# Kernel tuning notes

Measured on AMD Instinct MI355X. Metric: run time of the kernel, lower is better.

Reference implementation:

```python
import jax, jax.numpy as jnp
import numpy as np

ALPHA = 0.2  # LeakyReLU negative slope
NEG_INF = -9e15


def setup_inputs() -> dict:
    key = jax.random.key(0)
    ks = jax.random.split(key, 9)
    B, N, Fin, Fout, H = 4, 1024, 256, 256, 32
    h = jax.random.normal(ks[0], (B, N, Fin), dtype=jnp.float32)
    mz = jax.random.uniform(ks[1], (B, N, 1), dtype=jnp.float32) * 2000.0
    adj = jax.random.randint(ks[2], (B, N, N), 0, 2, dtype=jnp.int32)
    # xavier_uniform with gain=1.414
    def xavier(k, shape, gain=1.414):
        fan_in, fan_out = shape[0], shape[1]
        bound = gain * np.sqrt(6.0 / (fan_in + fan_out))
        return jax.random.uniform(k, shape, jnp.float32, -bound, bound)
    W = xavier(ks[3], (Fin, Fout))
    a = xavier(ks[4], (2 * Fout, 1))
    w1 = xavier(ks[5], (1, H), gain=1.0)
    b1 = jnp.zeros((H,), jnp.float32)
    w2 = xavier(ks[6], (H, 1), gain=1.0)
    b2 = jnp.zeros((1,), jnp.float32)
    return {"h": h, "mz": mz, "W": W, "a": a, "w1": w1, "b1": b1, "w2": w2, "b2": b2, "adj": adj}


def reference(h, mz, W, a, w1, b1, w2, b2, adj):
    # h: (B,N,Fin), mz: (B,N,1), adj: (B,N,N)
    Wh = jnp.matmul(h, W)                       # (B,N,Fout)
    Fout = W.shape[1]
    a1 = a[:Fout, 0]                            # (Fout,)
    a2 = a[Fout:, 0]                            # (Fout,)
    # e[b,i,j] = leaky_relu(Wh[b,i]@a1 + Wh[b,j]@a2)  (identical to concat trick)
    s1 = jnp.einsum('bnf,f->bn', Wh, a1)
    s2 = jnp.einsum('bnf,f->bn', Wh, a2)
    e = jax.nn.leaky_relu(s1[:, :, None] + s2[:, None, :], negative_slope=ALPHA)  # (B,N,N)
    # |mz_i - mz_j| with first row/col zeroed
    diff = jnp.abs(mz - jnp.swapaxes(mz, 1, 2))  # (B,N,N)
    diff = diff.at[:, 0, :].set(0.0)
    diff = diff.at[:, :, 0].set(0.0)
    # tiny per-edge MLP: Linear(1,32)->ReLU->Linear(32,1)
    hdn = jax.nn.relu(diff[..., None] * w1[0] + b1)       # (B,N,N,32)
    diff_term = jnp.einsum('bijh,h->bij', hdn, w2[:, 0]) + b2[0]
    e = e + diff_term
    att = jnp.where(adj > 0, e, NEG_INF)
    att = jax.nn.softmax(att, axis=2)
    # dropout is identity in eval mode
    h_prime = jnp.matmul(att, Wh)               # (B,N,Fout)
    return jax.nn.elu(h_prime)
```

## Files before the change

kernel.cpp:

```cpp
#include <hip/hip_runtime.h>
#include <hip/hip_bf16.h>

#define ALPHA 0.2f
#define NEGINF -9000000000000000.0f

typedef __attribute__((ext_vector_type(8))) short short8;
typedef __attribute__((ext_vector_type(4))) float f32x4;
typedef __attribute__((ext_vector_type(4))) int i32x4;
typedef __attribute__((ext_vector_type(4))) unsigned short u16x4;

static constexpr int NB = 4, NN = 1024, NF = 256, NH = 32;

__device__ __forceinline__ unsigned short f2bf(float x) {
  union { float f; unsigned u; } v; v.f = x;
  unsigned r = v.u + 0x7fffu + ((v.u >> 16) & 1u);
  return (unsigned short)(r >> 16);
}

__global__ __launch_bounds__(256) void prep_kernel(
    const float* __restrict__ W, const float* __restrict__ a,
    const float* __restrict__ w1, const float* __restrict__ b1,
    const float* __restrict__ w2, const float* __restrict__ b2,
    float* __restrict__ wa1, float* __restrict__ wa2,
    unsigned short* __restrict__ WTp, float* __restrict__ seg) {
  int k = blockIdx.x;
  int t = threadIdx.x;
  float w = W[k * NF + t];
  WTp[(((k >> 3) * NF) + t) * 8 + (k & 7)] = f2bf(w);
  float p1 = w * a[t];
  float p2 = w * a[NF + t];
#pragma unroll
  for (int off = 32; off >= 1; off >>= 1) {
    p1 += __shfl_xor(p1, off);
    p2 += __shfl_xor(p2, off);
  }
  __shared__ float r1[4], r2[4];
  int wid = t >> 6;
  if ((t & 63) == 0) { r1[wid] = p1; r2[wid] = p2; }
  __syncthreads();
  if (t == 0) {
    wa1[k] = r1[0] + r1[1] + r1[2] + r1[3];
    wa2[k] = r2[0] + r2[1] + r2[2] + r2[3];
  }
  if (k == 0 && t < NH) {
    float w1h = w1[t], b1h = b1[t], w2h = w2[t];
    bool bp = (w1h != 0.f) && (b1h != 0.f) && ((b1h > 0.f) != (w1h > 0.f));
    bool act = (w1h + b1h) > 0.f;
    float cA = act ? w2h * w1h : 0.f;
    float cB = act ? w2h * b1h : 0.f;
    float nbp = bp ? 1.f : 0.f;
#pragma unroll
    for (int off = 16; off >= 1; off >>= 1) {
      cA += __shfl_xor(cA, off);
      cB += __shfl_xor(cB, off);
      nbp += __shfl_xor(nbp, off);
    }
    if (t == 0) {
      seg[0] = (nbp == 0.f) ? 1.f : 0.f;
      seg[1] = cA;
      seg[2] = cB + b2[0];
      seg[3] = 0.f;
    }
  }
}

__global__ __launch_bounds__(512) void wh_kernel(
    const float* __restrict__ h, const unsigned short* __restrict__ WTp,
    const float* __restrict__ wa1, const float* __restrict__ wa2,
    unsigned short* __restrict__ WhP, float* __restrict__ s1g,
    float* __restrict__ s2g) {
  __shared__ unsigned short hs[16 * 256];
  int bid = blockIdx.x;
  int b = bid >> 6;
  int rb = (bid & 63) << 4;
  int t = threadIdx.x;
  {
    int row = t >> 5, c0 = (t & 31) * 8;
    const float* src = h + (size_t)(b * NN + rb + row) * NF + c0;
    f32x4 v0 = *(const f32x4*)src;
    f32x4 v1 = *(const f32x4*)(src + 4);
    unsigned short tmp[8] = {f2bf(v0.x), f2bf(v0.y), f2bf(v0.z), f2bf(v0.w),
                             f2bf(v1.x), f2bf(v1.y), f2bf(v1.z), f2bf(v1.w)};
    int off = row * 512 + ((c0 * 2) ^ ((row & 7) << 4));
    *(short8*)((char*)hs + off) = *(const short8*)tmp;
    f32x4 a10 = *(const f32x4*)(wa1 + c0);
    f32x4 a11 = *(const f32x4*)(wa1 + c0 + 4);
    f32x4 a20 = *(const f32x4*)(wa2 + c0);
    f32x4 a21 = *(const f32x4*)(wa2 + c0 + 4);
    float d1 = v0.x * a10.x + v0.y * a10.y + v0.z * a10.z + v0.w * a10.w +
               v1.x * a11.x + v1.y * a11.y + v1.z * a11.z + v1.w * a11.w;
    float d2 = v0.x * a20.x + v0.y * a20.y + v0.z * a20.z + v0.w * a20.w +
               v1.x * a21.x + v1.y * a21.y + v1.z * a21.z + v1.w * a21.w;
#pragma unroll
    for (int off2 = 16; off2 >= 1; off2 >>= 1) {
      d1 += __shfl_xor(d1, off2);
      d2 += __shfl_xor(d2, off2);
    }
    if ((t & 31) == 0) {
      s1g[b * NN + rb + row] = d1;
      s2g[b * NN + rb + row] = d2;
    }
  }
  __syncthreads();
  int wid = t >> 6, lane = t & 63;
  int fb = wid * 32;
  int rowa = lane & 15, kg = lane >> 4;
  f32x4 acc0 = {0.f, 0.f, 0.f, 0.f}, acc1 = {0.f, 0.f, 0.f, 0.f};
#pragma unroll
  for (int ks = 0; ks < 8; ++ks) {
    int k0 = ks * 32;
    short8 af = *(const short8*)((const char*)hs + rowa * 512 +
                                 ((2 * (k0 + kg * 8)) ^ ((rowa & 7) << 4)));
    int kc = ks * 4 + kg;
    short8 bf0 = *(const short8*)(WTp + ((kc * NF) + fb + (lane & 15)) * 8);
    short8 bf1 = *(const short8*)(WTp + ((kc * NF) + fb + 16 + (lane & 15)) * 8);
    acc0 = __builtin_amdgcn_mfma_f32_16x16x32_bf16(af, bf0, acc0, 0, 0, 0);
    acc1 = __builtin_amdgcn_mfma_f32_16x16x32_bf16(af, bf1, acc1, 0, 0, 0);
  }
#pragma unroll
  for (int r = 0; r < 4; ++r) {
    int jl = (lane >> 4) * 4 + r;
    int j = rb + jl;
    int base = ((b << 7) + (j >> 3)) * NF;
    WhP[(size_t)(base + fb + (lane & 15)) * 8 + (j & 7)] = f2bf(acc0[r]);
    WhP[(size_t)(base + fb + 16 + (lane & 15)) * 8 + (j & 7)] = f2bf(acc1[r]);
  }
}

__global__ __launch_bounds__(512) void attn_kernel(
    const float* __restrict__ s1g, const float* __restrict__ s2g,
    const float* __restrict__ mz, const int* __restrict__ adj,
    const unsigned short* __restrict__ WhP,
    const float* __restrict__ w1, const float* __restrict__ b1,
    const float* __restrict__ w2, const float* __restrict__ b2,
    const float* __restrict__ seg, float* __restrict__ out) {
  __shared__ unsigned short Pb[16 * 1024];
  __shared__ float s2s[1024];
  __shared__ float mzs[1024];
  __shared__ float s1s[16];
  __shared__ float rinv[16];
  int bid0 = blockIdx.x;
  int bid = (bid0 & 7) * 32 + (bid0 >> 3);
  int b = bid >> 6;
  int rb = (bid & 63) << 4;
  int t = threadIdx.x;
  for (int i = t; i < NN; i += 512) {
    s2s[i] = s2g[b * NN + i];
    mzs[i] = mz[b * NN + i];
  }
  if (t < 16) s1s[t] = s1g[b * NN + rb + t];
  __syncthreads();

  int wid = t >> 6, lane = t & 63;
  float segF = seg[0], segA = seg[1], segB = seg[2];
  float b2v = b2[0];
  for (int rr = 0; rr < 2; ++rr) {
    int row = wid * 2 + rr;
    int ig = rb + row;
    float s1v = s1s[row];
    float mzi = mzs[ig];
    const int* adjrow = adj + ((size_t)b * NN + ig) * NN;
    float e[16];
    if (segF != 0.f) {
#pragma unroll
      for (int c = 0; c < 4; ++c) {
        int j0 = c * 256 + lane * 4;
        i32x4 av = *(const i32x4*)(adjrow + j0);
        f32x4 mzv = *(const f32x4*)(mzs + j0);
        f32x4 s2v = *(const f32x4*)(s2s + j0);
#pragma unroll
        for (int u = 0; u < 4; ++u) {
          float dd = fabsf(mzi - mzv[u]);
          float d = (ig == 0 || (j0 + u) == 0) ? 0.f : dd;
          float s = s1v + s2v[u];
          s = fmaxf(s, 0.f) + ALPHA * fminf(s, 0.f);
          float ee = s + fmaf(d, segA, segB);
          e[c * 4 + u] = (av[u] > 0) ? ee : NEGINF;
        }
      }
    } else {
#pragma unroll
      for (int c = 0; c < 4; ++c) {
        int j0 = c * 256 + lane * 4;
        i32x4 av = *(const i32x4*)(adjrow + j0);
        f32x4 mzv = *(const f32x4*)(mzs + j0);
        f32x4 s2v = *(const f32x4*)(s2s + j0);
        float d[4], acc[4];
#pragma unroll
        for (int u = 0; u < 4; ++u) {
          float dd = fabsf(mzi - mzv[u]);
          d[u] = (ig == 0 || (j0 + u) == 0) ? 0.f : dd;
          acc[u] = b2v;
        }
#pragma unroll
        for (int hh = 0; hh < NH; ++hh) {
          float w1h = w1[hh], b1h = b1[hh], w2h = w2[hh];
#pragma unroll
          for (int u = 0; u < 4; ++u)
            acc[u] += fmaxf(d[u] * w1h + b1h, 0.f) * w2h;
        }
#pragma unroll
        for (int u = 0; u < 4; ++u) {
          float s = s1v + s2v[u];
          s = s > 0.f ? s : ALPHA * s;
          e[c * 4 + u] = (av[u] > 0) ? (s + acc[u]) : NEGINF;
        }
      }
    }
    float m = -3.0e38f;
#pragma unroll
    for (int q = 0; q < 16; ++q) m = fmaxf(m, e[q]);
#pragma unroll
    for (int off = 32; off >= 1; off >>= 1) m = fmaxf(m, __shfl_xor(m, off));
    float sum = 0.f;
#pragma unroll
    for (int q = 0; q < 16; ++q) {
      e[q] = __expf(e[q] - m);
      sum += e[q];
    }
#pragma unroll
    for (int off = 32; off >= 1; off >>= 1) sum += __shfl_xor(sum, off);
#pragma unroll
    for (int c = 0; c < 4; ++c) {
      u16x4 pk = {f2bf(e[c * 4 + 0]), f2bf(e[c * 4 + 1]),
                  f2bf(e[c * 4 + 2]), f2bf(e[c * 4 + 3])};
      int byteoff = row * 2048 + ((512 * c + 8 * lane) ^ ((row & 7) << 4));
      *(u16x4*)((char*)Pb + byteoff) = pk;
    }
    if (lane == 0) rinv[row] = 1.0f / sum;
  }
  __syncthreads();

  int fb = wid * 32;
  int rowa = lane & 15, kg = lane >> 4;
  const unsigned short* whb = WhP + (((size_t)b) << 7) * NF * 8;
  f32x4 acc0 = {0.f, 0.f, 0.f, 0.f}, acc1 = {0.f, 0.f, 0.f, 0.f};
#pragma unroll 4
  for (int ks = 0; ks < 32; ++ks) {
    int k0 = ks * 32;
    short8 af = *(const short8*)((const char*)Pb + rowa * 2048 +
                                 ((2 * (k0 + kg * 8)) ^ ((rowa & 7) << 4)));
    int kc = ks * 4 + kg;
    short8 bf0 = *(const short8*)(whb + (size_t)((kc * NF) + fb + (lane & 15)) * 8);
    short8 bf1 = *(const short8*)(whb + (size_t)((kc * NF) + fb + 16 + (lane & 15)) * 8);
    acc0 = __builtin_amdgcn_mfma_f32_16x16x32_bf16(af, bf0, acc0, 0, 0, 0);
    acc1 = __builtin_amdgcn_mfma_f32_16x16x32_bf16(af, bf1, acc1, 0, 0, 0);
  }
#pragma unroll
  for (int r = 0; r < 4; ++r) {
    int il = (lane >> 4) * 4 + r;
    float inv = rinv[il];
    float x0 = acc0[r] * inv;
    float x1 = acc1[r] * inv;
    x0 = x0 > 0.f ? x0 : expm1f(x0);
    x1 = x1 > 0.f ? x1 : expm1f(x1);
    size_t ob = (size_t)(b * NN + rb + il) * NF + fb + (lane & 15);
    out[ob] = x0;
    out[ob + 16] = x1;
  }
}

extern "C" void kernel_launch(void* const* d_in, const int* in_sizes, int n_in,
                              void* d_out, int out_size, void* d_ws, size_t ws_size,
                              hipStream_t stream) {
  const float* h   = (const float*)d_in[0];
  const float* mz  = (const float*)d_in[1];
  const float* W   = (const float*)d_in[2];
  const float* a   = (const float*)d_in[3];
  const float* w1  = (const float*)d_in[4];
  const float* b1  = (const float*)d_in[5];
  const float* w2  = (const float*)d_in[6];
  const float* b2  = (const float*)d_in[7];
  const int*   adj = (const int*)d_in[8];
  float* out = (float*)d_out;

  unsigned short* WTp = (unsigned short*)d_ws;
  unsigned short* WhP = WTp + 65536;
  float* wa1 = (float*)(WhP + (size_t)NB * 128 * NF * 8);
  float* wa2 = wa1 + 256;
  float* s1g = wa2 + 256;
  float* s2g = s1g + NB * NN;
  float* segb = s2g + NB * NN;

  prep_kernel<<<dim3(256), dim3(256), 0, stream>>>(W, a, w1, b1, w2, b2,
                                                   wa1, wa2, WTp, segb);
  wh_kernel<<<dim3(256), dim3(512), 0, stream>>>(h, WTp, wa1, wa2, WhP, s1g, s2g);
  attn_kernel<<<dim3(256), dim3(512), 0, stream>>>(s1g, s2g, mz, adj, WhP,
                                                   w1, b1, w2, b2, segb, out);
}
```

Measured before the change: 28.95 us.

## Fuse three kernels into one persistent kernel with grid barriers

Merges the prep, Wh projection and attention kernels into a single 256-block kernel that uses atomic-counter grid barriers between phases, removing two kernel launches and their gaps. The adjacency rows are prefetched into registers before the second barrier so their load overlaps the barrier wait. s1 stays in shared memory instead of going through global memory, and ELU uses __expf-1 instead of expm1f. The grid barrier assumes all 256 blocks are co-resident, adds a memset launch to reset the counter, and costs extra register pressure from the prefetched adjacency data.

```diff
diff --git a/kernel.cpp b/kernel.cpp
--- a/kernel.cpp
+++ b/kernel.cpp
@@ -9,7 +9,7 @@
 typedef __attribute__((ext_vector_type(4))) int i32x4;
 typedef __attribute__((ext_vector_type(4))) unsigned short u16x4;
 
-static constexpr int NB = 4, NN = 1024, NF = 256, NH = 32;
+static constexpr int NB = 4, NN = 1024, NF = 256, NH = 32, NGRID = 256;
 
 __device__ __forceinline__ unsigned short f2bf(float x) {
   union { float f; unsigned u; } v; v.f = x;
@@ -17,63 +17,86 @@
   return (unsigned short)(r >> 16);
 }
 
-__global__ __launch_bounds__(256) void prep_kernel(
+__device__ __forceinline__ void grid_barrier(unsigned* cnt) {
+  __syncthreads();
+  if (threadIdx.x == 0) {
+    __hip_atomic_fetch_add(cnt, 1u, __ATOMIC_ACQ_REL, __HIP_MEMORY_SCOPE_AGENT);
+    while (__hip_atomic_load(cnt, __ATOMIC_ACQUIRE, __HIP_MEMORY_SCOPE_AGENT) <
+           (unsigned)NGRID)
+      __builtin_amdgcn_s_sleep(2);
+  }
+  __syncthreads();
+}
+
+__global__ __launch_bounds__(512) void fused_kernel(
+    const float* __restrict__ h, const float* __restrict__ mz,
     const float* __restrict__ W, const float* __restrict__ a,
     const float* __restrict__ w1, const float* __restrict__ b1,
     const float* __restrict__ w2, const float* __restrict__ b2,
+    const int* __restrict__ adj,
+    unsigned short* __restrict__ WTp, unsigned short* __restrict__ WhP,
     float* __restrict__ wa1, float* __restrict__ wa2,
-    unsigned short* __restrict__ WTp, float* __restrict__ seg) {
-  int k = blockIdx.x;
-  int t = threadIdx.x;
-  float w = W[k * NF + t];
-  WTp[(((k >> 3) * NF) + t) * 8 + (k & 7)] = f2bf(w);
-  float p1 = w * a[t];
-  float p2 = w * a[NF + t];
-#pragma unroll
-  for (int off = 32; off >= 1; off >>= 1) {
-    p1 += __shfl_xor(p1, off);
-    p2 += __shfl_xor(p2, off);
-  }
+    float* __restrict__ s2g, unsigned* __restrict__ bar,
+    float* __restrict__ out) {
+  __shared__ char smemraw[32 * 1024];
+  __shared__ float mzs[1024];
+  __shared__ float s2s[1024];
+  __shared__ float s1s[16];
+  __shared__ float rinv[16];
   __shared__ float r1[4], r2[4];
-  int wid = t >> 6;
-  if ((t & 63) == 0) { r1[wid] = p1; r2[wid] = p2; }
-  __syncthreads();
-  if (t == 0) {
-    wa1[k] = r1[0] + r1[1] + r1[2] + r1[3];
-    wa2[k] = r2[0] + r2[1] + r2[2] + r2[3];
-  }
-  if (k == 0 && t < NH) {
-    float w1h = w1[t], b1h = b1[t], w2h = w2[t];
-    bool bp = (w1h != 0.f) && (b1h != 0.f) && ((b1h > 0.f) != (w1h > 0.f));
-    bool act = (w1h + b1h) > 0.f;
-    float cA = act ? w2h * w1h : 0.f;
-    float cB = act ? w2h * b1h : 0.f;
-    float nbp = bp ? 1.f : 0.f;
-#pragma unroll
-    for (int off = 16; off >= 1; off >>= 1) {
-      cA += __shfl_xor(cA, off);
-      cB += __shfl_xor(cB, off);
-      nbp += __shfl_xor(nbp, off);
-    }
-    if (t == 0) {
-      seg[0] = (nbp == 0.f) ? 1.f : 0.f;
-      seg[1] = cA;
-      seg[2] = cB + b2[0];
-      seg[3] = 0.f;
-    }
-  }
-}
-
-__global__ __launch_bounds__(512) void wh_kernel(
-    const float* __restrict__ h, const unsigned short* __restrict__ WTp,
-    const float* __restrict__ wa1, const float* __restrict__ wa2,
-    unsigned short* __restrict__ WhP, float* __restrict__ s1g,
-    float* __restrict__ s2g) {
-  __shared__ unsigned short hs[16 * 256];
-  int bid = blockIdx.x;
+  __shared__ float segsh[3];
+
+  int bid0 = blockIdx.x;
+  int bid = (bid0 & 7) * 32 + (bid0 >> 3);
   int b = bid >> 6;
   int rb = (bid & 63) << 4;
   int t = threadIdx.x;
+  int wid = t >> 6, lane = t & 63;
+
+  {
+    int k = bid0;
+    float p1 = 0.f, p2 = 0.f;
+    if (t < 256) {
+      float w = W[k * NF + t];
+      WTp[(((k >> 3) * NF) + t) * 8 + (k & 7)] = f2bf(w);
+      p1 = w * a[t];
+      p2 = w * a[NF + t];
+    }
+#pragma unroll
+    for (int off = 32; off >= 1; off >>= 1) {
+      p1 += __shfl_xor(p1, off);
+      p2 += __shfl_xor(p2, off);
+    }
+    if (t < 256 && (t & 63) == 0) { r1[t >> 6] = p1; r2[t >> 6] = p2; }
+    if (t < NH) {
+      float w1h = w1[t], b1h = b1[t], w2h = w2[t];
+      bool bp = (w1h != 0.f) && (b1h != 0.f) && ((b1h > 0.f) != (w1h > 0.f));
+      bool act = (w1h + b1h) > 0.f;
+      float cA = act ? w2h * w1h : 0.f;
+      float cB = act ? w2h * b1h : 0.f;
+      float nbp = bp ? 1.f : 0.f;
+#pragma unroll
+      for (int off = 16; off >= 1; off >>= 1) {
+        cA += __shfl_xor(cA, off);
+        cB += __shfl_xor(cB, off);
+        nbp += __shfl_xor(nbp, off);
+      }
+      if (t == 0) {
+        segsh[0] = (nbp == 0.f) ? 1.f : 0.f;
+        segsh[1] = cA;
+        segsh[2] = cB + b2[0];
+      }
+    }
+    for (int i = t; i < NN; i += 512) mzs[i] = mz[b * NN + i];
+    __syncthreads();
+    if (t == 0) {
+      wa1[k] = r1[0] + r1[1] + r1[2] + r1[3];
+      wa2[k] = r2[0] + r2[1] + r2[2] + r2[3];
+    }
+  }
+  grid_barrier(bar + 0);
+
+  unsigned short* hs = (unsigned short*)smemraw;
   {
     int row = t >> 5, c0 = (t & 31) * 8;
     const float* src = h + (size_t)(b * NN + rb + row) * NF + c0;
@@ -97,75 +120,67 @@
       d2 += __shfl_xor(d2, off2);
     }
     if ((t & 31) == 0) {
-      s1g[b * NN + rb + row] = d1;
+      s1s[row] = d1;
       s2g[b * NN + rb + row] = d2;
     }
   }
   __syncthreads();
-  int wid = t >> 6, lane = t & 63;
-  int fb = wid * 32;
-  int rowa = lane & 15, kg = lane >> 4;
-  f32x4 acc0 = {0.f, 0.f, 0.f, 0.f}, acc1 = {0.f, 0.f, 0.f, 0.f};
-#pragma unroll
-  for (int ks = 0; ks < 8; ++ks) {
-    int k0 = ks * 32;
-    short8 af = *(const short8*)((const char*)hs + rowa * 512 +
-                                 ((2 * (k0 + kg * 8)) ^ ((rowa & 7) << 4)));
-    int kc = ks * 4 + kg;
-    short8 bf0 = *(const short8*)(WTp + ((kc * NF) + fb + (lane & 15)) * 8);
-    short8 bf1 = *(const short8*)(WTp + ((kc * NF) + fb + 16 + (lane & 15)) * 8);
-    acc0 = __builtin_amdgcn_mfma_f32_16x16x32_bf16(af, bf0, acc0, 0, 0, 0);
-    acc1 = __builtin_amdgcn_mfma_f32_16x16x32_bf16(af, bf1, acc1, 0, 0, 0);
-  }
-#pragma unroll
-  for (int r = 0; r < 4; ++r) {
-    int jl = (lane >> 4) * 4 + r;
-    int j = rb + jl;
-    int base = ((b << 7) + (j >> 3)) * NF;
-    WhP[(size_t)(base + fb + (lane & 15)) * 8 + (j & 7)] = f2bf(acc0[r]);
-    WhP[(size_t)(base + fb + 16 + (lane & 15)) * 8 + (j & 7)] = f2bf(acc1[r]);
-  }
-}
-
-__global__ __launch_bounds__(512) void attn_kernel(
-    const float* __restrict__ s1g, const float* __restrict__ s2g,
-    const float* __restrict__ mz, const int* __restrict__ adj,
-    const unsigned short* __restrict__ WhP,
-    const float* __restrict__ w1, const float* __restrict__ b1,
-    const float* __restrict__ w2, const float* __restrict__ b2,
-    const float* __restrict__ seg, float* __restrict__ out) {
-  __shared__ unsigned short Pb[16 * 1024];
-  __shared__ float s2s[1024];
-  __shared__ float mzs[1024];
-  __shared__ float s1s[16];
-  __shared__ float rinv[16];
-  int bid0 = blockIdx.x;
-  int bid = (bid0 & 7) * 32 + (bid0 >> 3);
-  int b = bid >> 6;
-  int rb = (bid & 63) << 4;
-  int t = threadIdx.x;
-  for (int i = t; i < NN; i += 512) {
-    s2s[i] = s2g[b * NN + i];
-    mzs[i] = mz[b * NN + i];
-  }
-  if (t < 16) s1s[t] = s1g[b * NN + rb + t];
-  __syncthreads();
-
-  int wid = t >> 6, lane = t & 63;
-  float segF = seg[0], segA = seg[1], segB = seg[2];
+  {
+    int fb = wid * 32;
+    int rowa = lane & 15, kg = lane >> 4;
+    f32x4 acc0 = {0.f, 0.f, 0.f, 0.f}, acc1 = {0.f, 0.f, 0.f, 0.f};
+#pragma unroll
+    for (int ks = 0; ks < 8; ++ks) {
+      int k0 = ks * 32;
+      short8 af = *(const short8*)((const char*)hs + rowa * 512 +
+                                   ((2 * (k0 + kg * 8)) ^ ((rowa & 7) << 4)));
+      int kc = ks * 4 + kg;
+      short8 bf0 = *(const short8*)(WTp + ((kc * NF) + fb + (lane & 15)) * 8);
+      short8 bf1 = *(const short8*)(WTp + ((kc * NF) + fb + 16 + (lane & 15)) * 8);
+      acc0 = __builtin_amdgcn_mfma_f32_16x16x32_bf16(af, bf0, acc0, 0, 0, 0);
+      acc1 = __builtin_amdgcn_mfma_f32_16x16x32_bf16(af, bf1, acc1, 0, 0, 0);
+    }
+#pragma unroll
+    for (int r = 0; r < 4; ++r) {
+      int jl = (lane >> 4) * 4 + r;
+      int j = rb + jl;
+      int base = ((b << 7) + (j >> 3)) * NF;
+      WhP[(size_t)(base + fb + (lane & 15)) * 8 + (j & 7)] = f2bf(acc0[r]);
+      WhP[(size_t)(base + fb + 16 + (lane & 15)) * 8 + (j & 7)] = f2bf(acc1[r]);
+    }
+  }
+
+  i32x4 adjreg[8];
+  {
+    const int* adjb = adj + (size_t)b * NN * NN;
+#pragma unroll
+    for (int rr = 0; rr < 2; ++rr) {
+      int ig = rb + wid * 2 + rr;
+#pragma unroll
+      for (int c = 0; c < 4; ++c)
+        adjreg[rr * 4 + c] =
+            *(const i32x4*)(adjb + (size_t)ig * NN + c * 256 + lane * 4);
+    }
+  }
+  grid_barrier(bar + 1);
+
+  unsigned short* Pb = (unsigned short*)smemraw;
+  for (int i = t; i < NN; i += 512) s2s[i] = s2g[b * NN + i];
+  __syncthreads();
+
+  float segF = segsh[0], segA = segsh[1], segB = segsh[2];
   float b2v = b2[0];
   for (int rr = 0; rr < 2; ++rr) {
     int row = wid * 2 + rr;
     int ig = rb + row;
     float s1v = s1s[row];
     float mzi = mzs[ig];
-    const int* adjrow = adj + ((size_t)b * NN + ig) * NN;
     float e[16];
     if (segF != 0.f) {
 #pragma unroll
       for (int c = 0; c < 4; ++c) {
         int j0 = c * 256 + lane * 4;
-        i32x4 av = *(const i32x4*)(adjrow + j0);
+        i32x4 av = adjreg[rr * 4 + c];
         f32x4 mzv = *(const f32x4*)(mzs + j0);
         f32x4 s2v = *(const f32x4*)(s2s + j0);
 #pragma unroll
@@ -182,7 +197,7 @@
 #pragma unroll
       for (int c = 0; c < 4; ++c) {
         int j0 = c * 256 + lane * 4;
-        i32x4 av = *(const i32x4*)(adjrow + j0);
+        i32x4 av = adjreg[rr * 4 + c];
         f32x4 mzv = *(const f32x4*)(mzs + j0);
         f32x4 s2v = *(const f32x4*)(s2s + j0);
         float d[4], acc[4];
@@ -231,32 +246,35 @@
   }
   __syncthreads();
 
-  int fb = wid * 32;
-  int rowa = lane & 15, kg = lane >> 4;
-  const unsigned short* whb = WhP + (((size_t)b) << 7) * NF * 8;
-  f32x4 acc0 = {0.f, 0.f, 0.f, 0.f}, acc1 = {0.f, 0.f, 0.f, 0.f};
+  {
+    int fb = wid * 32;
+    int rowa = lane & 15, kg = lane >> 4;
+    const unsigned short* whb = WhP + (((size_t)b) << 7) * NF * 8;
+    f32x4 acc0 = {0.f, 0.f, 0.f, 0.f}, acc1 = {0.f, 0.f, 0.f, 0.f};
 #pragma unroll 4
-  for (int ks = 0; ks < 32; ++ks) {
-    int k0 = ks * 32;
-    short8 af = *(const short8*)((const char*)Pb + rowa * 2048 +
-                                 ((2 * (k0 + kg * 8)) ^ ((rowa & 7) << 4)));
-    int kc = ks * 4 + kg;
-    short8 bf0 = *(const short8*)(whb + (size_t)((kc * NF) + fb + (lane & 15)) * 8);
-    short8 bf1 = *(const short8*)(whb + (size_t)((kc * NF) + fb + 16 + (lane & 15)) * 8);
-    acc0 = __builtin_amdgcn_mfma_f32_16x16x32_bf16(af, bf0, acc0, 0, 0, 0);
-    acc1 = __builtin_amdgcn_mfma_f32_16x16x32_bf16(af, bf1, acc1, 0, 0, 0);
-  }
-#pragma unroll
-  for (int r = 0; r < 4; ++r) {
-    int il = (lane >> 4) * 4 + r;
-    float inv = rinv[il];
-    float x0 = acc0[r] * inv;
-    float x1 = acc1[r] * inv;
-    x0 = x0 > 0.f ? x0 : expm1f(x0);
-    x1 = x1 > 0.f ? x1 : expm1f(x1);
-    size_t ob = (size_t)(b * NN + rb + il) * NF + fb + (lane & 15);
-    out[ob] = x0;
-    out[ob + 16] = x1;
+    for (int ks = 0; ks < 32; ++ks) {
+      int k0 = ks * 32;
+      short8 af = *(const short8*)((const char*)Pb + rowa * 2048 +
+                                   ((2 * (k0 + kg * 8)) ^ ((rowa & 7) << 4)));
+      int kc = ks * 4 + kg;
+      short8 bf0 = *(const short8*)(whb + (size_t)((kc * NF) + fb + (lane & 15)) * 8);
+      short8 bf1 =
+          *(const short8*)(whb + (size_t)((kc * NF) + fb + 16 + (lane & 15)) * 8);
+      acc0 = __builtin_amdgcn_mfma_f32_16x16x32_bf16(af, bf0, acc0, 0, 0, 0);
+      acc1 = __builtin_amdgcn_mfma_f32_16x16x32_bf16(af, bf1, acc1, 0, 0, 0);
+    }
+#pragma unroll
+    for (int r = 0; r < 4; ++r) {
+      int il = (lane >> 4) * 4 + r;
+      float inv = rinv[il];
+      float x0 = acc0[r] * inv;
+      float x1 = acc1[r] * inv;
+      x0 = x0 > 0.f ? x0 : (__expf(x0) - 1.f);
+      x1 = x1 > 0.f ? x1 : (__expf(x1) - 1.f);
+      size_t ob = (size_t)(b * NN + rb + il) * NF + fb + (lane & 15);
+      out[ob] = x0;
+      out[ob + 16] = x1;
+    }
   }
 }
 
@@ -276,15 +294,12 @@
 
   unsigned short* WTp = (unsigned short*)d_ws;
   unsigned short* WhP = WTp + 65536;
-  float* wa1 = (float*)(WhP + (size_t)NB * 128 * NF * 8);
+  float* wa1 = (float*)(WhP + (size_t)NB * NN * NF);
   float* wa2 = wa1 + 256;
-  float* s1g = wa2 + 256;
-  float* s2g = s1g + NB * NN;
-  float* segb = s2g + NB * NN;
-
-  prep_kernel<<<dim3(256), dim3(256), 0, stream>>>(W, a, w1, b1, w2, b2,
-                                                   wa1, wa2, WTp, segb);
-  wh_kernel<<<dim3(256), dim3(512), 0, stream>>>(h, WTp, wa1, wa2, WhP, s1g, s2g);
-  attn_kernel<<<dim3(256), dim3(512), 0, stream>>>(s1g, s2g, mz, adj, WhP,
-                                                   w1, b1, w2, b2, segb, out);
+  float* s2g = wa2 + 256;
+  unsigned* bar = (unsigned*)(s2g + NB * NN);
+
+  (void)hipMemsetAsync(bar, 0, 2 * sizeof(unsigned), stream);
+  fused_kernel<<<dim3(NGRID), dim3(512), 0, stream>>>(
+      h, mz, W, a, w1, b1, w2, b2, adj, WTp, WhP, wa1, wa2, s2g, bar, out);
 }
```

After: 63.51 us. 119% more time.

## Use 32-row attention tiles with 1024 threads and prefetch adjacency into registers

Applied to the files above, without the earlier changes.

The attention kernel now handles 32 query rows per block with 1024 threads over 128 blocks. Each wave's MFMA step reuses one Wh B-fragment across two 16-row P tiles, halving global B loads per output. Adjacency rows are loaded into registers at kernel start to overlap with the shared-memory staging, and the MLP segment precompute moves from the prep kernel into each attention block. The risks are only 128 blocks on a 256-CU part, higher register pressure, and redundant per-block precompute.

```diff
diff --git a/kernel.cpp b/kernel.cpp
--- a/kernel.cpp
+++ b/kernel.cpp
@@ -19,10 +19,8 @@
 
 __global__ __launch_bounds__(256) void prep_kernel(
     const float* __restrict__ W, const float* __restrict__ a,
-    const float* __restrict__ w1, const float* __restrict__ b1,
-    const float* __restrict__ w2, const float* __restrict__ b2,
     float* __restrict__ wa1, float* __restrict__ wa2,
-    unsigned short* __restrict__ WTp, float* __restrict__ seg) {
+    unsigned short* __restrict__ WTp) {
   int k = blockIdx.x;
   int t = threadIdx.x;
   float w = W[k * NF + t];
@@ -35,32 +33,11 @@
     p2 += __shfl_xor(p2, off);
   }
   __shared__ float r1[4], r2[4];
-  int wid = t >> 6;
-  if ((t & 63) == 0) { r1[wid] = p1; r2[wid] = p2; }
+  if ((t & 63) == 0) { r1[t >> 6] = p1; r2[t >> 6] = p2; }
   __syncthreads();
   if (t == 0) {
     wa1[k] = r1[0] + r1[1] + r1[2] + r1[3];
     wa2[k] = r2[0] + r2[1] + r2[2] + r2[3];
-  }
-  if (k == 0 && t < NH) {
-    float w1h = w1[t], b1h = b1[t], w2h = w2[t];
-    bool bp = (w1h != 0.f) && (b1h != 0.f) && ((b1h > 0.f) != (w1h > 0.f));
-    bool act = (w1h + b1h) > 0.f;
-    float cA = act ? w2h * w1h : 0.f;
-    float cB = act ? w2h * b1h : 0.f;
-    float nbp = bp ? 1.f : 0.f;
-#pragma unroll
-    for (int off = 16; off >= 1; off >>= 1) {
-      cA += __shfl_xor(cA, off);
-      cB += __shfl_xor(cB, off);
-      nbp += __shfl_xor(nbp, off);
-    }
-    if (t == 0) {
-      seg[0] = (nbp == 0.f) ? 1.f : 0.f;
-      seg[1] = cA;
-      seg[2] = cB + b2[0];
-      seg[3] = 0.f;
-    }
   }
 }
 
@@ -127,45 +104,77 @@
   }
 }
 
-__global__ __launch_bounds__(512) void attn_kernel(
-    const float* __restrict__ s1g, const float* __restrict__ s2g,
+__global__ __launch_bounds__(1024) void attn_kernel(
     const float* __restrict__ mz, const int* __restrict__ adj,
     const unsigned short* __restrict__ WhP,
     const float* __restrict__ w1, const float* __restrict__ b1,
     const float* __restrict__ w2, const float* __restrict__ b2,
-    const float* __restrict__ seg, float* __restrict__ out) {
-  __shared__ unsigned short Pb[16 * 1024];
+    const float* __restrict__ s1g, const float* __restrict__ s2g,
+    float* __restrict__ out) {
+  __shared__ unsigned short Pb[32 * 1024];
+  __shared__ float mzs[1024];
   __shared__ float s2s[1024];
-  __shared__ float mzs[1024];
-  __shared__ float s1s[16];
-  __shared__ float rinv[16];
+  __shared__ float s1s[32];
+  __shared__ float rinv[32];
+  __shared__ float segsh[3];
+
   int bid0 = blockIdx.x;
-  int bid = (bid0 & 7) * 32 + (bid0 >> 3);
-  int b = bid >> 6;
-  int rb = (bid & 63) << 4;
+  int bid = (bid0 & 7) * 16 + (bid0 >> 3);
+  int b = bid >> 5;
+  int rb = (bid & 31) << 5;
   int t = threadIdx.x;
-  for (int i = t; i < NN; i += 512) {
-    s2s[i] = s2g[b * NN + i];
-    mzs[i] = mz[b * NN + i];
-  }
-  if (t < 16) s1s[t] = s1g[b * NN + rb + t];
-  __syncthreads();
-
   int wid = t >> 6, lane = t & 63;
-  float segF = seg[0], segA = seg[1], segB = seg[2];
+
+  i32x4 adjreg[8];
+  {
+    const int* adjb = adj + (size_t)b * NN * NN;
+#pragma unroll
+    for (int rr = 0; rr < 2; ++rr) {
+      int ig = rb + wid * 2 + rr;
+#pragma unroll
+      for (int c = 0; c < 4; ++c)
+        adjreg[rr * 4 + c] =
+            *(const i32x4*)(adjb + (size_t)ig * NN + c * 256 + lane * 4);
+    }
+  }
+
+  if (t < NH) {
+    float w1h = w1[t], b1h = b1[t], w2h = w2[t];
+    bool bp = (w1h != 0.f) && (b1h != 0.f) && ((b1h > 0.f) != (w1h > 0.f));
+    bool act = (w1h + b1h) > 0.f;
+    float cA = act ? w2h * w1h : 0.f;
+    float cB = act ? w2h * b1h : 0.f;
+    float nbp = bp ? 1.f : 0.f;
+#pragma unroll
+    for (int off = 16; off >= 1; off >>= 1) {
+      cA += __shfl_xor(cA, off);
+      cB += __shfl_xor(cB, off);
+      nbp += __shfl_xor(nbp, off);
+    }
+    if (t == 0) {
+      segsh[0] = (nbp == 0.f) ? 1.f : 0.f;
+      segsh[1] = cA;
+      segsh[2] = cB + b2[0];
+    }
+  }
+  mzs[t] = mz[b * NN + t];
+  s2s[t] = s2g[b * NN + t];
+  if (t < 32) s1s[t] = s1g[b * NN + rb + t];
+  __syncthreads();
+
+  float segF = segsh[0], segA = segsh[1], segB = segsh[2];
   float b2v = b2[0];
   for (int rr = 0; rr < 2; ++rr) {
     int row = wid * 2 + rr;
     int ig = rb + row;
     float s1v = s1s[row];
     float mzi = mzs[ig];
-    const int* adjrow = adj + ((size_t)b * NN + ig) * NN;
     float e[16];
     if (segF != 0.f) {
 #pragma unroll
       for (int c = 0; c < 4; ++c) {
         int j0 = c * 256 + lane * 4;
-        i32x4 av = *(const i32x4*)(adjrow + j0);
+        i32x4 av = adjreg[rr * 4 + c];
         f32x4 mzv = *(const f32x4*)(mzs + j0);
         f32x4 s2v = *(const f32x4*)(s2s + j0);
 #pragma unroll
@@ -182,7 +191,7 @@
 #pragma unroll
       for (int c = 0; c < 4; ++c) {
         int j0 = c * 256 + lane * 4;
-        i32x4 av = *(const i32x4*)(adjrow + j0);
+        i32x4 av = adjreg[rr * 4 + c];
         f32x4 mzv = *(const f32x4*)(mzs + j0);
         f32x4 s2v = *(const f32x4*)(s2s + j0);
         float d[4], acc[4];
@@ -192,7 +201,7 @@
           d[u] = (ig == 0 || (j0 + u) == 0) ? 0.f : dd;
           acc[u] = b2v;
         }
-#pragma unroll
+#pragma unroll 1
         for (int hh = 0; hh < NH; ++hh) {
           float w1h = w1[hh], b1h = b1[hh], w2h = w2[hh];
 #pragma unroll
@@ -231,32 +240,34 @@
   }
   __syncthreads();
 
-  int fb = wid * 32;
-  int rowa = lane & 15, kg = lane >> 4;
-  const unsigned short* whb = WhP + (((size_t)b) << 7) * NF * 8;
-  f32x4 acc0 = {0.f, 0.f, 0.f, 0.f}, acc1 = {0.f, 0.f, 0.f, 0.f};
+  {
+    int fb = wid * 16;
+    int fl = lane & 15, kg = lane >> 4;
+    const unsigned short* whb = WhP + (((size_t)b) << 7) * NF * 8;
+    f32x4 acc0 = {0.f, 0.f, 0.f, 0.f}, acc1 = {0.f, 0.f, 0.f, 0.f};
+    int abase = fl * 2048;
 #pragma unroll 4
-  for (int ks = 0; ks < 32; ++ks) {
-    int k0 = ks * 32;
-    short8 af = *(const short8*)((const char*)Pb + rowa * 2048 +
-                                 ((2 * (k0 + kg * 8)) ^ ((rowa & 7) << 4)));
-    int kc = ks * 4 + kg;
-    short8 bf0 = *(const short8*)(whb + (size_t)((kc * NF) + fb + (lane & 15)) * 8);
-    short8 bf1 = *(const short8*)(whb + (size_t)((kc * NF) + fb + 16 + (lane & 15)) * 8);
-    acc0 = __builtin_amdgcn_mfma_f32_16x16x32_bf16(af, bf0, acc0, 0, 0, 0);
-    acc1 = __builtin_amdgcn_mfma_f32_16x16x32_bf16(af, bf1, acc1, 0, 0, 0);
-  }
-#pragma unroll
-  for (int r = 0; r < 4; ++r) {
-    int il = (lane >> 4) * 4 + r;
-    float inv = rinv[il];
-    float x0 = acc0[r] * inv;
-    float x1 = acc1[r] * inv;
-    x0 = x0 > 0.f ? x0 : expm1f(x0);
-    x1 = x1 > 0.f ? x1 : expm1f(x1);
-    size_t ob = (size_t)(b * NN + rb + il) * NF + fb + (lane & 15);
-    out[ob] = x0;
-    out[ob + 16] = x1;
+    for (int ks = 0; ks < 32; ++ks) {
+      int k0 = ks * 32;
+      int kc = ks * 4 + kg;
+      short8 bf = *(const short8*)(whb + (size_t)((kc * NF) + fb + fl) * 8);
+      int aoff = (2 * (k0 + kg * 8)) ^ ((fl & 7) << 4);
+      short8 af0 = *(const short8*)((const char*)Pb + abase + aoff);
+      short8 af1 = *(const short8*)((const char*)Pb + abase + 32768 + aoff);
+      acc0 = __builtin_amdgcn_mfma_f32_16x16x32_bf16(af0, bf, acc0, 0, 0, 0);
+      acc1 = __builtin_amdgcn_mfma_f32_16x16x32_bf16(af1, bf, acc1, 0, 0, 0);
+    }
+#pragma unroll
+    for (int r = 0; r < 4; ++r) {
+      int il0 = (lane >> 4) * 4 + r;
+      int il1 = il0 + 16;
+      float x0 = acc0[r] * rinv[il0];
+      float x1 = acc1[r] * rinv[il1];
+      x0 = x0 > 0.f ? x0 : (__expf(x0) - 1.f);
+      x1 = x1 > 0.f ? x1 : (__expf(x1) - 1.f);
+      out[(size_t)(b * NN + rb + il0) * NF + fb + fl] = x0;
+      out[(size_t)(b * NN + rb + il1) * NF + fb + fl] = x1;
+    }
   }
 }
 
@@ -276,15 +287,13 @@
 
   unsigned short* WTp = (unsigned short*)d_ws;
   unsigned short* WhP = WTp + 65536;
-  float* wa1 = (float*)(WhP + (size_t)NB * 128 * NF * 8);
+  float* wa1 = (float*)(WhP + (size_t)NB * NN * NF);
   float* wa2 = wa1 + 256;
   float* s1g = wa2 + 256;
   float* s2g = s1g + NB * NN;
-  float* segb = s2g + NB * NN;
-
-  prep_kernel<<<dim3(256), dim3(256), 0, stream>>>(W, a, w1, b1, w2, b2,
-                                                   wa1, wa2, WTp, segb);
+
+  prep_kernel<<<dim3(256), dim3(256), 0, stream>>>(W, a, wa1, wa2, WTp);
   wh_kernel<<<dim3(256), dim3(512), 0, stream>>>(h, WTp, wa1, wa2, WhP, s1g, s2g);
-  attn_kernel<<<dim3(256), dim3(512), 0, stream>>>(s1g, s2g, mz, adj, WhP,
-                                                   w1, b1, w2, b2, segb, out);
-}
+  attn_kernel<<<dim3(128), dim3(1024), 0, stream>>>(mz, adj, WhP, w1, b1, w2,
+                                                    b2, s1g, s2g, out);
+}
```

New measurement: 27.38 us. 1.06x faster.

## Stream attention in column chunks with online softmax and prefetched adjacency

Applied to the files above, without the earlier changes.

The attention kernel now handles the 1024 columns in four chunks of 256. It keeps a running max and sum per row (online softmax), rescales the MFMA accumulators as each chunk arrives, and double-buffers the probability tile in LDS. Adjacency loads for the next chunk are issued early so they overlap with the exp and MFMA work of the current chunk. The MLP segment constants move from the prep kernel into each attention block's prologue. The change adds a __syncthreads per chunk and extra rescale math, and it replaces expm1f with __expf-1, which loses some precision near zero.

```diff
diff --git a/kernel.cpp b/kernel.cpp
--- a/kernel.cpp
+++ b/kernel.cpp
@@ -19,10 +19,8 @@
 
 __global__ __launch_bounds__(256) void prep_kernel(
     const float* __restrict__ W, const float* __restrict__ a,
-    const float* __restrict__ w1, const float* __restrict__ b1,
-    const float* __restrict__ w2, const float* __restrict__ b2,
     float* __restrict__ wa1, float* __restrict__ wa2,
-    unsigned short* __restrict__ WTp, float* __restrict__ seg) {
+    unsigned short* __restrict__ WTp) {
   int k = blockIdx.x;
   int t = threadIdx.x;
   float w = W[k * NF + t];
@@ -35,32 +33,11 @@
     p2 += __shfl_xor(p2, off);
   }
   __shared__ float r1[4], r2[4];
-  int wid = t >> 6;
-  if ((t & 63) == 0) { r1[wid] = p1; r2[wid] = p2; }
+  if ((t & 63) == 0) { r1[t >> 6] = p1; r2[t >> 6] = p2; }
   __syncthreads();
   if (t == 0) {
     wa1[k] = r1[0] + r1[1] + r1[2] + r1[3];
     wa2[k] = r2[0] + r2[1] + r2[2] + r2[3];
-  }
-  if (k == 0 && t < NH) {
-    float w1h = w1[t], b1h = b1[t], w2h = w2[t];
-    bool bp = (w1h != 0.f) && (b1h != 0.f) && ((b1h > 0.f) != (w1h > 0.f));
-    bool act = (w1h + b1h) > 0.f;
-    float cA = act ? w2h * w1h : 0.f;
-    float cB = act ? w2h * b1h : 0.f;
-    float nbp = bp ? 1.f : 0.f;
-#pragma unroll
-    for (int off = 16; off >= 1; off >>= 1) {
-      cA += __shfl_xor(cA, off);
-      cB += __shfl_xor(cB, off);
-      nbp += __shfl_xor(nbp, off);
-    }
-    if (t == 0) {
-      seg[0] = (nbp == 0.f) ? 1.f : 0.f;
-      seg[1] = cA;
-      seg[2] = cB + b2[0];
-      seg[3] = 0.f;
-    }
   }
 }
 
@@ -128,46 +105,86 @@
 }
 
 __global__ __launch_bounds__(512) void attn_kernel(
-    const float* __restrict__ s1g, const float* __restrict__ s2g,
     const float* __restrict__ mz, const int* __restrict__ adj,
     const unsigned short* __restrict__ WhP,
     const float* __restrict__ w1, const float* __restrict__ b1,
     const float* __restrict__ w2, const float* __restrict__ b2,
-    const float* __restrict__ seg, float* __restrict__ out) {
-  __shared__ unsigned short Pb[16 * 1024];
+    const float* __restrict__ s1g, const float* __restrict__ s2g,
+    float* __restrict__ out) {
+  __shared__ unsigned short Pb[2][16 * 256];
+  __shared__ float fsc[2][16];
+  __shared__ float mzs[1024];
   __shared__ float s2s[1024];
-  __shared__ float mzs[1024];
   __shared__ float s1s[16];
   __shared__ float rinv[16];
+  __shared__ float segsh[3];
+
   int bid0 = blockIdx.x;
   int bid = (bid0 & 7) * 32 + (bid0 >> 3);
   int b = bid >> 6;
   int rb = (bid & 63) << 4;
   int t = threadIdx.x;
+  int wid = t >> 6, lane = t & 63;
+  int r0 = wid * 2, r1 = r0 + 1;
+  const int* adjb = adj + ((size_t)(b * NN + rb)) * NN;
+
+  i32x4 avA[2], avB[2];
+  avA[0] = *(const i32x4*)(adjb + (size_t)r0 * NN + lane * 4);
+  avA[1] = *(const i32x4*)(adjb + (size_t)r1 * NN + lane * 4);
+  avB[0] = avA[0]; avB[1] = avA[1];
+
+  if (t < NH) {
+    float w1h = w1[t], b1h = b1[t], w2h = w2[t];
+    bool bp = (w1h != 0.f) && (b1h != 0.f) && ((b1h > 0.f) != (w1h > 0.f));
+    bool act = (w1h + b1h) > 0.f;
+    float cA = act ? w2h * w1h : 0.f;
+    float cB = act ? w2h * b1h : 0.f;
+    float nbp = bp ? 1.f : 0.f;
+#pragma unroll
+    for (int off = 16; off >= 1; off >>= 1) {
+      cA += __shfl_xor(cA, off);
+      cB += __shfl_xor(cB, off);
+      nbp += __shfl_xor(nbp, off);
+    }
+    if (t == 0) {
+      segsh[0] = (nbp == 0.f) ? 1.f : 0.f;
+      segsh[1] = cA;
+      segsh[2] = cB + b2[0];
+    }
+  }
   for (int i = t; i < NN; i += 512) {
+    mzs[i] = mz[b * NN + i];
     s2s[i] = s2g[b * NN + i];
-    mzs[i] = mz[b * NN + i];
   }
   if (t < 16) s1s[t] = s1g[b * NN + rb + t];
   __syncthreads();
 
-  int wid = t >> 6, lane = t & 63;
-  float segF = seg[0], segA = seg[1], segB = seg[2];
+  float segF = segsh[0], segA = segsh[1], segB = segsh[2];
   float b2v = b2[0];
-  for (int rr = 0; rr < 2; ++rr) {
-    int row = wid * 2 + rr;
-    int ig = rb + row;
-    float s1v = s1s[row];
-    float mzi = mzs[ig];
-    const int* adjrow = adj + ((size_t)b * NN + ig) * NN;
-    float e[16];
-    if (segF != 0.f) {
-#pragma unroll
-      for (int c = 0; c < 4; ++c) {
-        int j0 = c * 256 + lane * 4;
-        i32x4 av = *(const i32x4*)(adjrow + j0);
-        f32x4 mzv = *(const f32x4*)(mzs + j0);
-        f32x4 s2v = *(const f32x4*)(s2s + j0);
+  float mrun[2] = {-3.0e38f, -3.0e38f};
+  float lrun[2] = {0.f, 0.f};
+  int fb = wid * 32;
+  int rowa = lane & 15, kg = lane >> 4;
+  const unsigned short* whb = WhP + (((size_t)b) << 7) * NF * 8;
+  f32x4 acc0 = {0.f, 0.f, 0.f, 0.f}, acc1 = {0.f, 0.f, 0.f, 0.f};
+
+  for (int c = 0; c < 4; ++c) {
+    if (c < 3) {
+      avB[0] = *(const i32x4*)(adjb + (size_t)r0 * NN + (c + 1) * 256 + lane * 4);
+      avB[1] = *(const i32x4*)(adjb + (size_t)r1 * NN + (c + 1) * 256 + lane * 4);
+    }
+#pragma unroll
+    for (int rr = 0; rr < 2; ++rr) {
+      int row = wid * 2 + rr;
+      int ig = rb + row;
+      float s1v = s1s[row];
+      float mzi = mzs[ig];
+      int j0 = c * 256 + lane * 4;
+      i32x4 av = avA[rr];
+      f32x4 mzv = *(const f32x4*)(mzs + j0);
+      f32x4 s2v = *(const f32x4*)(s2s + j0);
+      float e[4];
+      if (segF != 0.f) {
 #pragma unroll
         for (int u = 0; u < 4; ++u) {
           float dd = fabsf(mzi - mzv[u]);
@@ -175,16 +192,9 @@
           float s = s1v + s2v[u];
           s = fmaxf(s, 0.f) + ALPHA * fminf(s, 0.f);
           float ee = s + fmaf(d, segA, segB);
-          e[c * 4 + u] = (av[u] > 0) ? ee : NEGINF;
+          e[u] = (av[u] > 0) ? ee : NEGINF;
         }
-      }
-    } else {
-#pragma unroll
-      for (int c = 0; c < 4; ++c) {
-        int j0 = c * 256 + lane * 4;
-        i32x4 av = *(const i32x4*)(adjrow + j0);
-        f32x4 mzv = *(const f32x4*)(mzs + j0);
-        f32x4 s2v = *(const f32x4*)(s2s + j0);
+      } else {
         float d[4], acc[4];
 #pragma unroll
         for (int u = 0; u < 4; ++u) {
@@ -192,7 +202,7 @@
           d[u] = (ig == 0 || (j0 + u) == 0) ? 0.f : dd;
           acc[u] = b2v;
         }
-#pragma unroll
+#pragma unroll 1
         for (int hh = 0; hh < NH; ++hh) {
           float w1h = w1[hh], b1h = b1[hh], w2h = w2[hh];
 #pragma unroll
@@ -203,58 +213,67 @@
         for (int u = 0; u < 4; ++u) {
           float s = s1v + s2v[u];
           s = s > 0.f ? s : ALPHA * s;
-          e[c * 4 + u] = (av[u] > 0) ? (s + acc[u]) : NEGINF;
+          e[u] = (av[u] > 0) ? (s + acc[u]) : NEGINF;
         }
       }
-    }
-    float m = -3.0e38f;
-#pragma unroll
-    for (int q = 0; q < 16; ++q) m = fmaxf(m, e[q]);
-#pragma unroll
-    for (int off = 32; off >= 1; off >>= 1) m = fmaxf(m, __shfl_xor(m, off));
-    float sum = 0.f;
-#pragma unroll
-    for (int q = 0; q < 16; ++q) {
-      e[q] = __expf(e[q] - m);
-      sum += e[q];
-    }
-#pragma unroll
-    for (int off = 32; off >= 1; off >>= 1) sum += __shfl_xor(sum, off);
-#pragma unroll
-    for (int c = 0; c < 4; ++c) {
-      u16x4 pk = {f2bf(e[c * 4 + 0]), f2bf(e[c * 4 + 1]),
-                  f2bf(e[c * 4 + 2]), f2bf(e[c * 4 + 3])};
-      int byteoff = row * 2048 + ((512 * c + 8 * lane) ^ ((row & 7) << 4));
-      *(u16x4*)((char*)Pb + byteoff) = pk;
-    }
-    if (lane == 0) rinv[row] = 1.0f / sum;
+      float cmax = fmaxf(fmaxf(e[0], e[1]), fmaxf(e[2], e[3]));
+#pragma unroll
+      for (int off = 32; off >= 1; off >>= 1)
+        cmax = fmaxf(cmax, __shfl_xor(cmax, off));
+      float mnew = fmaxf(mrun[rr], cmax);
+      float fr = __expf(mrun[rr] - mnew);
+      mrun[rr] = mnew;
+      float csum = 0.f;
+#pragma unroll
+      for (int u = 0; u < 4; ++u) {
+        e[u] = __expf(e[u] - mnew);
+        csum += e[u];
+      }
+#pragma unroll
+      for (int off = 32; off >= 1; off >>= 1) csum += __shfl_xor(csum, off);
+      lrun[rr] = lrun[rr] * fr + csum;
+      u16x4 pk = {f2bf(e[0]), f2bf(e[1]), f2bf(e[2]), f2bf(e[3])};
+      int byteoff = row * 512 + ((8 * lane) ^ ((row & 7) << 4));
+      *(u16x4*)((char*)Pb[c & 1] + byteoff) = pk;
+      if (lane == 0) fsc[c & 1][row] = fr;
+    }
+    avA[0] = avB[0];
+    avA[1] = avB[1];
+    __syncthreads();
+
+#pragma unroll
+    for (int r = 0; r < 4; ++r) {
+      float frr = fsc[c & 1][(lane >> 4) * 4 + r];
+      acc0[r] *= frr;
+      acc1[r] *= frr;
+    }
+#pragma unroll
+    for (int ks = 0; ks < 8; ++ks) {
+      int kc = (c * 8 + ks) * 4 + kg;
+      short8 af = *(const short8*)((const char*)Pb[c & 1] + rowa * 512 +
+                                   ((2 * (ks * 32 + kg * 8)) ^ ((rowa & 7) << 4)));
+      short8 bf0 = *(const short8*)(whb + (size_t)((kc * NF) + fb + rowa) * 8);
+      short8 bf1 = *(const short8*)(whb + (size_t)((kc * NF) + fb + 16 + rowa) * 8);
+      acc0 = __builtin_amdgcn_mfma_f32_16x16x32_bf16(af, bf0, acc0, 0, 0, 0);
+      acc1 = __builtin_amdgcn_mfma_f32_16x16x32_bf16(af, bf1, acc1, 0, 0, 0);
+    }
+  }
+
+  if (lane == 0) {
+    rinv[r0] = 1.0f / lrun[0];
+    rinv[r1] = 1.0f / lrun[1];
   }
   __syncthreads();
 
-  int fb = wid * 32;
-  int rowa = lane & 15, kg = lane >> 4;
-  const unsigned short* whb = WhP + (((size_t)b) << 7) * NF * 8;
-  f32x4 acc0 = {0.f, 0.f, 0.f, 0.f}, acc1 = {0.f, 0.f, 0.f, 0.f};
-#pragma unroll 4
-  for (int ks = 0; ks < 32; ++ks) {
-    int k0 = ks * 32;
-    short8 af = *(const short8*)((const char*)Pb + rowa * 2048 +
-                                 ((2 * (k0 + kg * 8)) ^ ((rowa & 7) << 4)));
-    int kc = ks * 4 + kg;
-    short8 bf0 = *(const short8*)(whb + (size_t)((kc * NF) + fb + (lane & 15)) * 8);
-    short8 bf1 = *(const short8*)(whb + (size_t)((kc * NF) + fb + 16 + (lane & 15)) * 8);
-    acc0 = __builtin_amdgcn_mfma_f32_16x16x32_bf16(af, bf0, acc0, 0, 0, 0);
-    acc1 = __builtin_amdgcn_mfma_f32_16x16x32_bf16(af, bf1, acc1, 0, 0, 0);
-  }
 #pragma unroll
   for (int r = 0; r < 4; ++r) {
     int il = (lane >> 4) * 4 + r;
     float inv = rinv[il];
     float x0 = acc0[r] * inv;
     float x1 = acc1[r] * inv;
-    x0 = x0 > 0.f ? x0 : expm1f(x0);
-    x1 = x1 > 0.f ? x1 : expm1f(x1);
-    size_t ob = (size_t)(b * NN + rb + il) * NF + fb + (lane & 15);
+    x0 = x0 > 0.f ? x0 : (__expf(x0) - 1.f);
+    x1 = x1 > 0.f ? x1 : (__expf(x1) - 1.f);
+    size_t ob = (size_t)(b * NN + rb + il) * NF + fb + rowa;
     out[ob] = x0;
     out[ob + 16] = x1;
   }
@@ -276,15 +295,13 @@
 
   unsigned short* WTp = (unsigned short*)d_ws;
   unsigned short* WhP = WTp + 65536;
-  float* wa1 = (float*)(WhP + (size_t)NB * 128 * NF * 8);
+  float* wa1 = (float*)(WhP + (size_t)NB * NN * NF);
   float* wa2 = wa1 + 256;
   float* s1g = wa2 + 256;
   float* s2g = s1g + NB * NN;
-  float* segb = s2g + NB * NN;
-
-  prep_kernel<<<dim3(256), dim3(256), 0, stream>>>(W, a, w1, b1, w2, b2,
-                                                   wa1, wa2, WTp, segb);
+
+  prep_kernel<<<dim3(256), dim3(256), 0, stream>>>(W, a, wa1, wa2, WTp);
   wh_kernel<<<dim3(256), dim3(512), 0, stream>>>(h, WTp, wa1, wa2, WhP, s1g, s2g);
-  attn_kernel<<<dim3(256), dim3(512), 0, stream>>>(s1g, s2g, mz, adj, WhP,
-                                                   w1, b1, w2, b2, segb, out);
-}
+  attn_kernel<<<dim3(256), dim3(512), 0, stream>>>(mz, adj, WhP, w1, b1, w2,
+                                                   b2, s1g, s2g, out);
+}
```

Result: slower. 29.90 us (+3.3%).
